# Performance work log

Measured on AMD Instinct MI355X. Metric: run time of the kernel, lower is better.

The kernel has to match this reference:

```python
import jax, jax.numpy as jnp
import numpy as np

B, T, D, H = 4, 2048, 512, 8
K = D // H  # head dim = 64

def setup_inputs() -> dict:
    key = jax.random.key(0)
    k1, k2, k3, k4 = jax.random.split(key, 4)
    x = jax.random.normal(k1, (B, T, D), dtype=jnp.float32)
    # torch nn.Linear stores weight as [out_features, in_features]
    w_qkv = jax.random.normal(k2, (3 * D, D), dtype=jnp.float32) * (D ** -0.5)
    w_proj = jax.random.normal(k3, (D, D), dtype=jnp.float32) * (D ** -0.5)
    b_proj = jax.random.normal(k4, (D,), dtype=jnp.float32) * 0.01
    return {"x": x, "w_qkv": w_qkv, "w_proj": w_proj, "b_proj": b_proj}

def reference(x, w_qkv, w_proj, b_proj):
    Bx, Tx, Dx = x.shape
    # qkv projection (no bias): [B,T,3D]
    qkv = jnp.einsum('btd,ed->bte', x, w_qkv)
    q, k, v = jnp.split(qkv, 3, axis=-1)
    # [B,H,T,K]
    def heads(t):
        return t.reshape(Bx, Tx, H, K).transpose(0, 2, 1, 3)
    q, k, v = heads(q), heads(k), heads(v)
    # scaled scores with causal mask
    scores = jnp.einsum('bhqk,bhsk->bhqs', q, k) * (K ** -0.5)  # [B,H,T,T]
    causal = jnp.tril(jnp.ones((Tx, Tx), dtype=bool))
    scores = jnp.where(causal, scores, -jnp.inf)
    attn = jax.nn.softmax(scores, axis=-1)  # dropout p=0.0 -> identity
    out = jnp.einsum('bhqs,bhsk->bhqk', attn, v)  # [B,H,T,K]
    out = out.transpose(0, 2, 1, 3).reshape(Bx, Tx, Dx)
    out = jnp.einsum('btd,ed->bte', out, w_proj) + b_proj
    return out
```

## Files before the change

kernel.cpp:

```cpp
#include <hip/hip_runtime.h>


typedef unsigned short u16;
typedef __attribute__((ext_vector_type(8))) __bf16 bf16x8;
typedef __attribute__((ext_vector_type(8))) unsigned short u16x8;
typedef __attribute__((ext_vector_type(4))) float f32x4;

#define DEV static __device__ __forceinline__

DEV void async16(const u16* g, u16* l) {
  __builtin_amdgcn_global_load_lds(
      (const __attribute__((address_space(1))) unsigned int*)g,
      (__attribute__((address_space(3))) unsigned int*)l, 16, 0, 0);
}
DEV u16x8 gld8(const u16* p) { return *(const u16x8*)p; }
DEV void lst8(u16* p, u16x8 v) { *(u16x8*)p = v; }
DEV bf16x8 ldsld8(const u16* p) {
  return __builtin_bit_cast(bf16x8, *(const u16x8*)p);
}
DEV f32x4 mfma16(bf16x8 a, bf16x8 b, f32x4 c) {
  return __builtin_amdgcn_mfma_f32_16x16x32_bf16(a, b, c, 0, 0, 0);
}
DEV u16 f2b(float f) {
  unsigned u = __builtin_bit_cast(unsigned, f);
  u += 0x7FFFu + ((u >> 16) & 1u);
  return (u16)(u >> 16);
}
DEV u16x8 pack8(f32x4 a, f32x4 b) {
  u16x8 r;
  r[0] = f2b(a[0]); r[1] = f2b(a[1]); r[2] = f2b(a[2]); r[3] = f2b(a[3]);
  r[4] = f2b(b[0]); r[5] = f2b(b[1]); r[6] = f2b(b[2]); r[7] = f2b(b[3]);
  return r;
}

__global__ void cvt_all(const float* __restrict__ x, const float* __restrict__ wq,
                        u16* __restrict__ xb, u16* __restrict__ wqb) {
  constexpr long NX = 8192L * 512 / 8;
  constexpr long NQ = 1536L * 512 / 8;
  const long i = (long)blockIdx.x * 256 + threadIdx.x;
  if (i < NX) {
    const float* p = x + i * 8;
    *(u16x8*)(xb + i * 8) = pack8(*(const f32x4*)p, *(const f32x4*)(p + 4));
  } else if (i < NX + NQ) {
    const long j = i - NX;
    const float* p = wq + j * 8;
    *(u16x8*)(wqb + j * 8) = pack8(*(const f32x4*)p, *(const f32x4*)(p + 4));
  }
}

__global__ void gemm_bb(const u16* __restrict__ A, const u16* __restrict__ Bt,
                        u16* __restrict__ C, int N, int K) {
  __shared__ __align__(16) u16 As[2][128 * 32];
  __shared__ __align__(16) u16 Bs[2][128 * 32];

  const int t = threadIdx.x, lane = t & 63, w = t >> 6;
  const int lane15 = lane & 15, quad = lane >> 4;
  const int wr = w >> 1, wc = w & 1;
  const long row0 = (long)blockIdx.y * 128;
  const int col0 = blockIdx.x * 128;

  const int srow = w * 16 + (lane >> 2);
  const int scol = (lane & 3) * 8;
  const u16* Ag = A + (row0 + srow) * (long)K + scol;
  const u16* Bg = Bt + ((long)col0 + srow) * (long)K + scol;

  f32x4 acc[4][4];
#pragma unroll
  for (int i = 0; i < 4; i++)
#pragma unroll
    for (int j = 0; j < 4; j++) acc[i][j] = (f32x4)(0.0f);

  for (int k0 = 0; k0 < K; k0 += 64) {
    __syncthreads();
#pragma unroll
    for (int r = 0; r < 2; r++) {
#pragma unroll
      for (int hf = 0; hf < 2; hf++) {
        async16(Ag + (long)r * 64 * K + k0 + hf * 32,
                &As[hf][(r * 64 + w * 16) * 32]);
        async16(Bg + (long)r * 64 * K + k0 + hf * 32,
                &Bs[hf][(r * 64 + w * 16) * 32]);
      }
    }
    __syncthreads();

#pragma unroll
    for (int hf = 0; hf < 2; hf++) {
      bf16x8 a[4], b[4];
#pragma unroll
      for (int i = 0; i < 4; i++)
        a[i] = ldsld8(&As[hf][(wr * 64 + i * 16 + lane15) * 32 + quad * 8]);
#pragma unroll
      for (int j = 0; j < 4; j++)
        b[j] = ldsld8(&Bs[hf][(wc * 64 + j * 16 + lane15) * 32 + quad * 8]);
#pragma unroll
      for (int i = 0; i < 4; i++)
#pragma unroll
        for (int j = 0; j < 4; j++) acc[i][j] = mfma16(a[i], b[j], acc[i][j]);
    }
  }

#pragma unroll
  for (int i = 0; i < 4; i++)
#pragma unroll
    for (int j = 0; j < 4; j++) {
      const int col = col0 + wc * 64 + j * 16 + lane15;
#pragma unroll
      for (int r = 0; r < 4; r++) {
        const long row = row0 + wr * 64 + i * 16 + quad * 4 + r;
        C[row * (long)N + col] = f2b(acc[i][j][r]);
      }
    }
}

__global__ void gemm_b64(const u16* __restrict__ A, const float* __restrict__ Bt,
                         const float* __restrict__ bias, float* __restrict__ C,
                         int N, int K) {
  __shared__ __align__(16) u16 As[2][128 * 32];
  __shared__ __align__(16) u16 Bs[2][64 * 32];

  const int t = threadIdx.x, lane = t & 63, w = t >> 6;
  const int lane15 = lane & 15, quad = lane >> 4;
  const int wr = w >> 1, wc = w & 1;
  const long row0 = (long)blockIdx.y * 128;
  const int col0 = blockIdx.x * 64;

  const int srow = w * 16 + (lane >> 2);
  const int scol = (lane & 3) * 8;
  const u16* Ag = A + (row0 + srow) * (long)K + scol;

  const int brow = t >> 2, bc = (t & 3) * 16;
  const float* Bg = Bt + (long)(col0 + brow) * K + bc;
  u16* BsD = &Bs[bc >> 5][brow * 32 + (bc & 31)];

  f32x4 acc[4][2];
#pragma unroll
  for (int i = 0; i < 4; i++)
#pragma unroll
    for (int j = 0; j < 2; j++) acc[i][j] = (f32x4)(0.0f);

  f32x4 q0 = *(const f32x4*)Bg, q1 = *(const f32x4*)(Bg + 4);
  f32x4 q2 = *(const f32x4*)(Bg + 8), q3 = *(const f32x4*)(Bg + 12);

  for (int k0 = 0; k0 < K; k0 += 64) {
    __syncthreads();
#pragma unroll
    for (int r = 0; r < 2; r++)
#pragma unroll
      for (int hf = 0; hf < 2; hf++)
        async16(Ag + (long)r * 64 * K + k0 + hf * 32,
                &As[hf][(r * 64 + w * 16) * 32]);
    lst8(BsD, pack8(q0, q1));
    lst8(BsD + 8, pack8(q2, q3));
    __syncthreads();

    {
      const int kp = (k0 + 64 < K) ? k0 + 64 : k0;
      q0 = *(const f32x4*)(Bg + kp);     q1 = *(const f32x4*)(Bg + kp + 4);
      q2 = *(const f32x4*)(Bg + kp + 8); q3 = *(const f32x4*)(Bg + kp + 12);
    }

#pragma unroll
    for (int hf = 0; hf < 2; hf++) {
      bf16x8 a[4], b[2];
#pragma unroll
      for (int i = 0; i < 4; i++)
        a[i] = ldsld8(&As[hf][(wr * 64 + i * 16 + lane15) * 32 + quad * 8]);
#pragma unroll
      for (int j = 0; j < 2; j++)
        b[j] = ldsld8(&Bs[hf][(wc * 32 + j * 16 + lane15) * 32 + quad * 8]);
#pragma unroll
      for (int i = 0; i < 4; i++)
#pragma unroll
        for (int j = 0; j < 2; j++) acc[i][j] = mfma16(a[i], b[j], acc[i][j]);
    }
  }

#pragma unroll
  for (int i = 0; i < 4; i++)
#pragma unroll
    for (int j = 0; j < 2; j++) {
      const int col = col0 + wc * 32 + j * 16 + lane15;
      const float bv = bias[col];
#pragma unroll
      for (int r = 0; r < 4; r++) {
        const long row = row0 + wr * 64 + i * 16 + quad * 4 + r;
        C[row * (long)N + col] = acc[i][j][r] + bv;
      }
    }
}

__global__ void attn_v3(const u16* __restrict__ qkv, u16* __restrict__ out) {
  constexpr int T = 2048, LD = 1536;
  constexpr float CEXP = 0.18033688f;
  __shared__ __align__(16) u16 Ks[64 * 72];
  __shared__ __align__(16) u16 Vt[64 * 72];
  __shared__ __align__(16) u16 Ps[4][16 * 72];

  const int t = threadIdx.x, lane = t & 63, w = t >> 6;
  const int lane15 = lane & 15, quad = lane >> 4;

  const int i = blockIdx.x;
  int qb = i & 31;
  if (i >= 512) qb = 31 - qb;
  const int h = (i >> 5) & 7;
  const int b = (i >> 8) & 3;
  const long base = (long)b * T * LD;

  const u16* gq =
      qkv + base + (long)(qb * 64 + w * 16 + lane15) * LD + h * 64 + quad * 8;
  const bf16x8 qa0 = __builtin_bit_cast(bf16x8, *(const u16x8*)gq);
  const bf16x8 qa1 = __builtin_bit_cast(bf16x8, *(const u16x8*)(gq + 32));

  const int srow = t >> 3, sc8 = (t & 7) * 8;
  const int vs = t >> 2, vd0 = (t & 3) * 16;

  const int nsb = qb + 1;

  u16x8 kr0, kr1, vr0, vr1;
  {
    const u16* gk = qkv + base + (long)srow * LD + 512 + h * 64 + sc8;
    const u16* gv = qkv + base + (long)vs * LD + 1024 + h * 64 + vd0;
    kr0 = gld8(gk); kr1 = gld8(gk + (long)32 * LD);
    vr0 = gld8(gv); vr1 = gld8(gv + 8);
  }

  float lp[4] = {0.0f, 0.0f, 0.0f, 0.0f};
  f32x4 o[4];
#pragma unroll
  for (int j = 0; j < 4; j++) o[j] = (f32x4)(0.0f);

  const int qrow_base = qb * 64 + w * 16 + quad * 4;

  for (int sb = 0; sb < nsb; ++sb) {
    __syncthreads();
    lst8(&Ks[srow * 72 + sc8], kr0);
    lst8(&Ks[(srow + 32) * 72 + sc8], kr1);
#pragma unroll
    for (int ii = 0; ii < 8; ii++) {
      const int d = vd0 + ii;
      Vt[d * 72 + (vs ^ (((d >> 3) & 7) << 3))] = vr0[ii];
    }
#pragma unroll
    for (int ii = 0; ii < 8; ii++) {
      const int d = vd0 + 8 + ii;
      Vt[d * 72 + (vs ^ (((d >> 3) & 7) << 3))] = vr1[ii];
    }
    __syncthreads();

    {
      const int sp = (sb + 1 < nsb) ? sb + 1 : sb;
      const u16* gk = qkv + base + (long)(sp * 64 + srow) * LD + 512 + h * 64 + sc8;
      const u16* gv = qkv + base + (long)(sp * 64 + vs) * LD + 1024 + h * 64 + vd0;
      kr0 = gld8(gk); kr1 = gld8(gk + (long)32 * LD);
      vr0 = gld8(gv); vr1 = gld8(gv + 8);
    }

    f32x4 sf[4];
#pragma unroll
    for (int j = 0; j < 4; j++) {
      f32x4 z = (f32x4)(0.0f);
      z = mfma16(qa0, ldsld8(&Ks[(j * 16 + lane15) * 72 + quad * 8]), z);
      sf[j] = mfma16(qa1, ldsld8(&Ks[(j * 16 + lane15) * 72 + quad * 8 + 32]), z);
    }

    if (sb == qb) {
      const int scol_base = sb * 64 + lane15;
#pragma unroll
      for (int j = 0; j < 4; j++)
#pragma unroll
        for (int r = 0; r < 4; r++) {
          float p = exp2f(sf[j][r] * CEXP);
          if (scol_base + j * 16 > qrow_base + r) p = 0.0f;
          sf[j][r] = p;
          lp[r] += p;
        }
    } else {
#pragma unroll
      for (int j = 0; j < 4; j++)
#pragma unroll
        for (int r = 0; r < 4; r++) {
          const float p = exp2f(sf[j][r] * CEXP);
          sf[j][r] = p;
          lp[r] += p;
        }
    }

    u16* myP = Ps[w];
#pragma unroll
    for (int j = 0; j < 4; j++)
#pragma unroll
      for (int r = 0; r < 4; r++)
        myP[(quad * 4 + r) * 72 + j * 16 + lane15] = f2b(sf[j][r]);
    __asm__ __volatile__("" ::: "memory");
    const bf16x8 pa0 = ldsld8(&myP[lane15 * 72 + quad * 8]);
    const bf16x8 pa1 = ldsld8(&myP[lane15 * 72 + quad * 8 + 32]);
    __asm__ __volatile__("" ::: "memory");

#pragma unroll
    for (int j = 0; j < 4; j++) {
      const int d0 = j * 16 + lane15;
      const int swz = ((d0 >> 3) & 7) << 3;
      o[j] = mfma16(pa0, ldsld8(&Vt[d0 * 72 + ((quad * 8) ^ swz)]), o[j]);
      o[j] = mfma16(pa1, ldsld8(&Vt[d0 * 72 + ((quad * 8 + 32) ^ swz)]), o[j]);
    }
  }

#pragma unroll
  for (int off = 1; off < 16; off <<= 1)
#pragma unroll
    for (int r = 0; r < 4; r++) lp[r] += __shfl_xor(lp[r], off);

  const long orow0 = (long)b * T + qb * 64 + w * 16;
  float inv[4];
#pragma unroll
  for (int r = 0; r < 4; r++) inv[r] = 1.0f / lp[r];
#pragma unroll
  for (int j = 0; j < 4; j++)
#pragma unroll
    for (int r = 0; r < 4; r++)
      out[(orow0 + quad * 4 + r) * 512 + h * 64 + j * 16 + lane15] =
          f2b(o[j][r] * inv[r]);
}

extern "C" void kernel_launch(void* const* d_in, const int* in_sizes, int n_in,
                              void* d_out, int out_size, void* d_ws, size_t ws_size,
                              hipStream_t stream) {
  const float* x      = (const float*)d_in[0];
  const float* w_qkv  = (const float*)d_in[1];
  const float* w_proj = (const float*)d_in[2];
  const float* b_proj = (const float*)d_in[3];
  float* out = (float*)d_out;

  u16* qkv = (u16*)d_ws;
  u16* xb  = qkv + (size_t)8192 * 1536;
  u16* wqb = (u16*)d_out;

  cvt_all<<<2432, 256, 0, stream>>>(x, w_qkv, xb, wqb);
  gemm_bb<<<dim3(12, 64), 256, 0, stream>>>(xb, wqb, qkv, 1536, 512);
  attn_v3<<<1024, 256, 0, stream>>>(qkv, xb);
  gemm_b64<<<dim3(8, 64), 256, 0, stream>>>(xb, w_proj, b_proj, out, 512, 512);
}
```

Before: 163.8 us.

## Fold softmax scale into Q epilogue, packed bf16 convert, remap GEMM block order

Three separate changes. The softmax scale-times-log2e factor is multiplied into the Q columns in the QKV GEMM epilogue, which removes a multiply per score in the attention kernel. Float-to-bf16 packing now uses the HIP paired conversion intrinsic instead of manual bit rounding. Both GEMMs switch to a 1D grid with a remapped tile order. Rounding Q to bf16 after scaling slightly changes numerics, and the new tile order changes which blocks run at the same time, which may affect L2 reuse.

```diff
diff --git a/kernel.cpp b/kernel.cpp
--- a/kernel.cpp
+++ b/kernel.cpp
@@ -1,10 +1,12 @@
 #include <hip/hip_runtime.h>
+#include <hip/hip_bf16.h>
 
 
 typedef unsigned short u16;
 typedef __attribute__((ext_vector_type(8))) __bf16 bf16x8;
 typedef __attribute__((ext_vector_type(8))) unsigned short u16x8;
 typedef __attribute__((ext_vector_type(4))) float f32x4;
+typedef __attribute__((ext_vector_type(4))) unsigned u32x4;
 
 #define DEV static __device__ __forceinline__
 
@@ -26,11 +28,19 @@
   u += 0x7FFFu + ((u >> 16) & 1u);
   return (u16)(u >> 16);
 }
+DEV unsigned pk2(float x, float y) {
+  __hip_bfloat162 t = __float22bfloat162_rn(float2{x, y});
+  unsigned r;
+  __builtin_memcpy(&r, &t, 4);
+  return r;
+}
 DEV u16x8 pack8(f32x4 a, f32x4 b) {
-  u16x8 r;
-  r[0] = f2b(a[0]); r[1] = f2b(a[1]); r[2] = f2b(a[2]); r[3] = f2b(a[3]);
-  r[4] = f2b(b[0]); r[5] = f2b(b[1]); r[6] = f2b(b[2]); r[7] = f2b(b[3]);
-  return r;
+  u32x4 t;
+  t[0] = pk2(a[0], a[1]);
+  t[1] = pk2(a[2], a[3]);
+  t[2] = pk2(b[0], b[1]);
+  t[3] = pk2(b[2], b[3]);
+  return __builtin_bit_cast(u16x8, t);
 }
 
 __global__ void cvt_all(const float* __restrict__ x, const float* __restrict__ wq,
@@ -56,8 +66,12 @@
   const int t = threadIdx.x, lane = t & 63, w = t >> 6;
   const int lane15 = lane & 15, quad = lane >> 4;
   const int wr = w >> 1, wc = w & 1;
-  const long row0 = (long)blockIdx.y * 128;
-  const int col0 = blockIdx.x * 128;
+
+  const int i = blockIdx.x;
+  const int rt = (i & 7) | (((i >> 3) & 7) << 3);
+  const int ct = i >> 6;
+  const long row0 = (long)rt * 128;
+  const int col0 = ct * 128;
 
   const int srow = w * 16 + (lane >> 2);
   const int scol = (lane & 3) * 8;
@@ -66,14 +80,14 @@
 
   f32x4 acc[4][4];
 #pragma unroll
-  for (int i = 0; i < 4; i++)
-#pragma unroll
-    for (int j = 0; j < 4; j++) acc[i][j] = (f32x4)(0.0f);
+  for (int ii = 0; ii < 4; ii++)
+#pragma unroll
+    for (int j = 0; j < 4; j++) acc[ii][j] = (f32x4)(0.0f);
 
   for (int k0 = 0; k0 < K; k0 += 64) {
     __syncthreads();
 #pragma unroll
-    for (int r = 0; r < 2; r++) {
+    for (int r = 0; r < 2; r++)
 #pragma unroll
       for (int hf = 0; hf < 2; hf++) {
         async16(Ag + (long)r * 64 * K + k0 + hf * 32,
@@ -81,34 +95,34 @@
         async16(Bg + (long)r * 64 * K + k0 + hf * 32,
                 &Bs[hf][(r * 64 + w * 16) * 32]);
       }
-    }
     __syncthreads();
 
 #pragma unroll
     for (int hf = 0; hf < 2; hf++) {
       bf16x8 a[4], b[4];
 #pragma unroll
-      for (int i = 0; i < 4; i++)
-        a[i] = ldsld8(&As[hf][(wr * 64 + i * 16 + lane15) * 32 + quad * 8]);
+      for (int ii = 0; ii < 4; ii++)
+        a[ii] = ldsld8(&As[hf][(wr * 64 + ii * 16 + lane15) * 32 + quad * 8]);
 #pragma unroll
       for (int j = 0; j < 4; j++)
         b[j] = ldsld8(&Bs[hf][(wc * 64 + j * 16 + lane15) * 32 + quad * 8]);
 #pragma unroll
-      for (int i = 0; i < 4; i++)
-#pragma unroll
-        for (int j = 0; j < 4; j++) acc[i][j] = mfma16(a[i], b[j], acc[i][j]);
-    }
-  }
-
-#pragma unroll
-  for (int i = 0; i < 4; i++)
+      for (int ii = 0; ii < 4; ii++)
+#pragma unroll
+        for (int j = 0; j < 4; j++) acc[ii][j] = mfma16(a[ii], b[j], acc[ii][j]);
+    }
+  }
+
+#pragma unroll
+  for (int ii = 0; ii < 4; ii++)
 #pragma unroll
     for (int j = 0; j < 4; j++) {
       const int col = col0 + wc * 64 + j * 16 + lane15;
+      const float sc = (col < 512) ? 0.18033688f : 1.0f;
 #pragma unroll
       for (int r = 0; r < 4; r++) {
-        const long row = row0 + wr * 64 + i * 16 + quad * 4 + r;
-        C[row * (long)N + col] = f2b(acc[i][j][r]);
+        const long row = row0 + wr * 64 + ii * 16 + quad * 4 + r;
+        C[row * (long)N + col] = f2b(acc[ii][j][r] * sc);
       }
     }
 }
@@ -122,8 +136,12 @@
   const int t = threadIdx.x, lane = t & 63, w = t >> 6;
   const int lane15 = lane & 15, quad = lane >> 4;
   const int wr = w >> 1, wc = w & 1;
-  const long row0 = (long)blockIdx.y * 128;
-  const int col0 = blockIdx.x * 64;
+
+  const int i = blockIdx.x;
+  const int rt = (i & 7) | (((i >> 3) & 7) << 3);
+  const int ct = i >> 6;
+  const long row0 = (long)rt * 128;
+  const int col0 = ct * 64;
 
   const int srow = w * 16 + (lane >> 2);
   const int scol = (lane & 3) * 8;
@@ -135,9 +153,9 @@
 
   f32x4 acc[4][2];
 #pragma unroll
-  for (int i = 0; i < 4; i++)
-#pragma unroll
-    for (int j = 0; j < 2; j++) acc[i][j] = (f32x4)(0.0f);
+  for (int ii = 0; ii < 4; ii++)
+#pragma unroll
+    for (int j = 0; j < 2; j++) acc[ii][j] = (f32x4)(0.0f);
 
   f32x4 q0 = *(const f32x4*)Bg, q1 = *(const f32x4*)(Bg + 4);
   f32x4 q2 = *(const f32x4*)(Bg + 8), q3 = *(const f32x4*)(Bg + 12);
@@ -164,35 +182,34 @@
     for (int hf = 0; hf < 2; hf++) {
       bf16x8 a[4], b[2];
 #pragma unroll
-      for (int i = 0; i < 4; i++)
-        a[i] = ldsld8(&As[hf][(wr * 64 + i * 16 + lane15) * 32 + quad * 8]);
+      for (int ii = 0; ii < 4; ii++)
+        a[ii] = ldsld8(&As[hf][(wr * 64 + ii * 16 + lane15) * 32 + quad * 8]);
 #pragma unroll
       for (int j = 0; j < 2; j++)
         b[j] = ldsld8(&Bs[hf][(wc * 32 + j * 16 + lane15) * 32 + quad * 8]);
 #pragma unroll
-      for (int i = 0; i < 4; i++)
-#pragma unroll
-        for (int j = 0; j < 2; j++) acc[i][j] = mfma16(a[i], b[j], acc[i][j]);
-    }
-  }
-
-#pragma unroll
-  for (int i = 0; i < 4; i++)
+      for (int ii = 0; ii < 4; ii++)
+#pragma unroll
+        for (int j = 0; j < 2; j++) acc[ii][j] = mfma16(a[ii], b[j], acc[ii][j]);
+    }
+  }
+
+#pragma unroll
+  for (int ii = 0; ii < 4; ii++)
 #pragma unroll
     for (int j = 0; j < 2; j++) {
       const int col = col0 + wc * 32 + j * 16 + lane15;
       const float bv = bias[col];
 #pragma unroll
       for (int r = 0; r < 4; r++) {
-        const long row = row0 + wr * 64 + i * 16 + quad * 4 + r;
-        C[row * (long)N + col] = acc[i][j][r] + bv;
+        const long row = row0 + wr * 64 + ii * 16 + quad * 4 + r;
+        C[row * (long)N + col] = acc[ii][j][r] + bv;
       }
     }
 }
 
 __global__ void attn_v3(const u16* __restrict__ qkv, u16* __restrict__ out) {
   constexpr int T = 2048, LD = 1536;
-  constexpr float CEXP = 0.18033688f;
   __shared__ __align__(16) u16 Ks[64 * 72];
   __shared__ __align__(16) u16 Vt[64 * 72];
   __shared__ __align__(16) u16 Ps[4][16 * 72];
@@ -270,7 +287,7 @@
       for (int j = 0; j < 4; j++)
 #pragma unroll
         for (int r = 0; r < 4; r++) {
-          float p = exp2f(sf[j][r] * CEXP);
+          float p = exp2f(sf[j][r]);
           if (scol_base + j * 16 > qrow_base + r) p = 0.0f;
           sf[j][r] = p;
           lp[r] += p;
@@ -280,7 +297,7 @@
       for (int j = 0; j < 4; j++)
 #pragma unroll
         for (int r = 0; r < 4; r++) {
-          const float p = exp2f(sf[j][r] * CEXP);
+          const float p = exp2f(sf[j][r]);
           sf[j][r] = p;
           lp[r] += p;
         }
@@ -337,7 +354,7 @@
   u16* wqb = (u16*)d_out;
 
   cvt_all<<<2432, 256, 0, stream>>>(x, w_qkv, xb, wqb);
-  gemm_bb<<<dim3(12, 64), 256, 0, stream>>>(xb, wqb, qkv, 1536, 512);
+  gemm_bb<<<768, 256, 0, stream>>>(xb, wqb, qkv, 1536, 512);
   attn_v3<<<1024, 256, 0, stream>>>(qkv, xb);
-  gemm_b64<<<dim3(8, 64), 256, 0, stream>>>(xb, w_proj, b_proj, out, 512, 512);
-}
+  gemm_b64<<<512, 256, 0, stream>>>(xb, w_proj, b_proj, out, 512, 512);
+}
```

New measurement: 160.9 us. No clear change (-1.7%).
